# Performance work log

Hardware: AMD Instinct MI355X
Metric: run time of the kernel (lower is better)

## Reference

```python
import jax, jax.numpy as jnp
import numpy as np

H, DK, DV = 16, 64, 64
DECAY = 0.99
WRITE_STRENGTH = 1.0


def setup_inputs() -> dict:
    key = jax.random.key(0)
    ks = jax.random.split(key, 7)
    B, S, D = 4, 4096, 2048
    sd = 1.0 / np.sqrt(D)
    return {
        "hidden": jax.random.normal(ks[0], (B, S, D), jnp.float32),
        "memory": jax.random.normal(ks[1], (H, DK, DV), jnp.float32) * 0.02,
        "Wk": jax.random.normal(ks[2], (H * DK, D), jnp.float32) * sd,
        "Wv": jax.random.normal(ks[3], (H * DV, D), jnp.float32) * sd,
        "Wq": jax.random.normal(ks[4], (H * DK, D), jnp.float32) * sd,
        "Wg": jax.random.normal(ks[5], (D, D), jnp.float32) * sd,
        "Wo": jax.random.normal(ks[6], (D, H * DV), jnp.float32) * (1.0 / np.sqrt(H * DV)),
    }


def reference(hidden, memory, Wk, Wv, Wq, Wg, Wo):
    B, S, D = hidden.shape
    # projections (Linear, bias=False): x @ W^T
    k = (hidden @ Wk.T).reshape(B, S, H, DK)
    v = (hidden @ Wv.T).reshape(B, S, H, DV)
    q = (hidden @ Wq.T).reshape(B, S, H, DK)
    # read with pre-update memory: r = q^T M
    readout = jnp.einsum('bshk,hkv->bshv', q, memory).reshape(B, S, H * DV)
    # output gate: h' = h + sigmoid(Wg h) * (Wo r)
    gate = jax.nn.sigmoid(hidden @ Wg.T)
    out = hidden + gate * (readout @ Wo.T)
    # decaying outer-product write: M' = lambda*M + rho * sum_i k_i v_i^T
    new_memory = DECAY * memory + WRITE_STRENGTH * jnp.einsum('bshk,bshv->hkv', k, v)
    return out, new_memory
```

## Files before the change

kernel.cpp:

```cpp
#include <hip/hip_runtime.h>
#include <hip/hip_bf16.h>

typedef __attribute__((ext_vector_type(4))) float f32x4;
typedef __bf16 bf16x8 __attribute__((ext_vector_type(8)));

#define TOKENS 16384
#define DIM    2048
#define NKVQ   3072

__device__ __forceinline__ void gload_lds16(const void* g, void* l) {
  __builtin_amdgcn_global_load_lds((const __attribute__((address_space(1))) void*)g,
                                   (__attribute__((address_space(3))) void*)l, 16, 0, 0);
}

__device__ __forceinline__ unsigned short bfbits(float x) {
  __bf16 b = (__bf16)x; return __builtin_bit_cast(unsigned short, b);
}

__global__ void cast8_kernel(const float* __restrict__ src, __bf16* __restrict__ dst, int n8) {
  int i = blockIdx.x * blockDim.x + threadIdx.x;
  if (i >= n8) return;
  const float4* s = (const float4*)src;
  float4 a = s[2 * i], b = s[2 * i + 1];
  bf16x8 o;
  o[0] = (__bf16)a.x; o[1] = (__bf16)a.y; o[2] = (__bf16)a.z; o[3] = (__bf16)a.w;
  o[4] = (__bf16)b.x; o[5] = (__bf16)b.y; o[6] = (__bf16)b.z; o[7] = (__bf16)b.w;
  ((bf16x8*)dst)[i] = o;
}

__global__ void weff_kernel(const float* __restrict__ Wo, const float* __restrict__ mem,
                            __bf16* __restrict__ Weff) {
  int idx = blockIdx.x * blockDim.x + threadIdx.x;
  int d = idx >> 10, hk = idx & 1023, h = hk >> 6;
  const float* wo = Wo + d * 1024 + h * 64;
  const float* mm = mem + hk * 64;
  float s = 0.f;
  #pragma unroll 8
  for (int v = 0; v < 64; ++v) s += wo[v] * mm[v];
  Weff[idx] = (__bf16)s;
}

__device__ __forceinline__ void gemm256_core(
    const __bf16* __restrict__ A, int lda,
    const __bf16* __restrict__ B, int ldb,
    int m0, int n0, int nt, char* sm, f32x4 acc[8][4]) {

  const int tid = threadIdx.x, lane = tid & 63, wid = tid >> 6;
  const int wr = wid >> 2, wc = wid & 3;
  const int lrow = lane & 15, kc = lane >> 4;

  int offA[8], offB[4];
  #pragma unroll
  for (int m = 0; m < 8; ++m) {
    int u = (wr * 128 + m * 16 + lrow) * 4 + kc;
    offA[m] = (u ^ ((u >> 3) & 7)) << 4;
  }
  #pragma unroll
  for (int n = 0; n < 4; ++n) {
    int u = (wc * 64 + n * 16 + lrow) * 4 + kc;
    offB[n] = ((u ^ ((u >> 3) & 7)) << 4) + 16384;
  }

  const __bf16* pSA[2]; const __bf16* pSB[2];
  #pragma unroll
  for (int s = 0; s < 2; ++s) {
    int U = s * 512 + tid;
    int u = U ^ ((U >> 3) & 7);
    pSA[s] = A + (size_t)(m0 + (u >> 2)) * lda + (u & 3) * 8;
    pSB[s] = B + (size_t)(n0 + (u >> 2)) * ldb + (u & 3) * 8;
  }

  bf16x8 bvS0[4], bvS1[4];

#define BARX() asm volatile("s_barrier" ::: "memory")
#define VM4()  asm volatile("s_waitcnt vmcnt(4)" ::: "memory")
#define VM0()  asm volatile("s_waitcnt vmcnt(0)" ::: "memory")
#define NOVM
#define NOSTAGE
#define STAGE(bb, tt) do { \
    char* sA = sm + (bb) * 32768 + tid * 16; \
    gload_lds16(pSA[0] + (tt) * 32, sA); \
    gload_lds16(pSA[1] + (tt) * 32, sA + 8192); \
    gload_lds16(pSB[0] + (tt) * 32, sA + 16384); \
    gload_lds16(pSB[1] + (tt) * 32, sA + 24576); } while (0)

#define PH(bufC, bufN, C, N, STG, WT) do { \
    const char* bC = sm + (bufC) * 32768; \
    const char* bN = sm + (bufN) * 32768; \
    bf16x8 av[8]; \
    _Pragma("unroll") for (int m = 0; m < 8; ++m) av[m] = *(const bf16x8*)(bC + offA[m]); \
    _Pragma("unroll") for (int n = 0; n < 4; ++n) bvS##N[n] = *(const bf16x8*)(bN + offB[n]); \
    STG; \
    __builtin_amdgcn_s_setprio(1); \
    _Pragma("unroll") for (int m = 0; m < 8; ++m) \
      _Pragma("unroll") for (int n = 0; n < 4; ++n) \
        acc[m][n] = __builtin_amdgcn_mfma_f32_16x16x32_bf16(av[m], bvS##C[n], acc[m][n], 0, 0, 0); \
    __builtin_amdgcn_s_setprio(0); \
    WT; BARX(); } while (0)

#define PHF(bufC, C) do { \
    const char* bC = sm + (bufC) * 32768; \
    bf16x8 av[8]; \
    _Pragma("unroll") for (int m = 0; m < 8; ++m) av[m] = *(const bf16x8*)(bC + offA[m]); \
    __builtin_amdgcn_s_setprio(1); \
    _Pragma("unroll") for (int m = 0; m < 8; ++m) \
      _Pragma("unroll") for (int n = 0; n < 4; ++n) \
        acc[m][n] = __builtin_amdgcn_mfma_f32_16x16x32_bf16(av[m], bvS##C[n], acc[m][n], 0, 0, 0); \
    __builtin_amdgcn_s_setprio(0); } while (0)

  STAGE(0, 0); STAGE(1, 1); STAGE(2, 2);
  VM4(); BARX();
  #pragma unroll
  for (int n = 0; n < 4; ++n) bvS0[n] = *(const bf16x8*)(sm + offB[n]);

  for (int i = 0, e = (nt - 4) >> 2; i < e; ++i) {
    const int t = i << 2;
    PH(0, 1, 0, 1, STAGE(3, t + 3), VM4());
    PH(1, 2, 1, 0, STAGE(0, t + 4), VM4());
    PH(2, 3, 0, 1, STAGE(1, t + 5), VM4());
    PH(3, 0, 1, 0, STAGE(2, t + 6), VM4());
  }
  PH(0, 1, 0, 1, STAGE(3, nt - 1), VM4());
  PH(1, 2, 1, 0, NOSTAGE, VM0());
  PH(2, 3, 0, 1, NOSTAGE, NOVM);
  PHF(3, 1);
#undef PH
#undef PHF
#undef STAGE
#undef BARX
#undef VM4
#undef VM0
#undef NOVM
#undef NOSTAGE
}

__global__ void __launch_bounds__(512, 1)
gemm_fused_kernel(const __bf16* __restrict__ Xb, const __bf16* __restrict__ W1,
                  __bf16* __restrict__ Y, __bf16* __restrict__ Gb) {
  __shared__ __attribute__((aligned(16))) char smem[131072];
  const int g = (blockIdx.x & 7) * 160 + (blockIdx.x >> 3);
  const int bm = g / 20, bn = g % 20;
  const int m0 = bm * 256, n0 = bn * 256;
  f32x4 acc[8][4] = {};
  gemm256_core(Xb, DIM, W1, DIM, m0, n0, 64, smem, acc);

  const int tid = threadIdx.x, wid = tid >> 6, lane = tid & 63;
  const int wr = wid >> 2, wc = wid & 3;
  const int crow = (lane >> 4) << 2, ccol = lane & 15;
  if (bn < 12) {
    #pragma unroll
    for (int f = 0; f < 8; ++f) {
      int row = m0 + wr * 128 + f * 16 + crow;
      #pragma unroll
      for (int n = 0; n < 4; ++n) {
        int col = n0 + wc * 64 + n * 16 + ccol;
        #pragma unroll
        for (int j = 0; j < 4; ++j)
          __builtin_nontemporal_store(bfbits(acc[f][n][j]),
              (unsigned short*)(Y + (size_t)(row + j) * NKVQ + col));
      }
    }
  } else {
    const int c0 = n0 - 3072;
    #pragma unroll
    for (int f = 0; f < 8; ++f) {
      int row = m0 + wr * 128 + f * 16 + crow;
      #pragma unroll
      for (int n = 0; n < 4; ++n) {
        int col = c0 + wc * 64 + n * 16 + ccol;
        #pragma unroll
        for (int j = 0; j < 4; ++j) {
          float gv = 1.0f / (1.0f + __expf(-acc[f][n][j]));
          __builtin_nontemporal_store(bfbits(gv),
              (unsigned short*)(Gb + (size_t)(row + j) * DIM + col));
        }
      }
    }
  }
}

__global__ void __launch_bounds__(512, 1)
gemm_read_kernel(const __bf16* __restrict__ Yq, const __bf16* __restrict__ Weff,
                 const __bf16* __restrict__ Gb, const float* __restrict__ hidden,
                 float* __restrict__ out) {
  __shared__ __attribute__((aligned(16))) char smem[131072];
  const int g = (blockIdx.x & 7) * 64 + (blockIdx.x >> 3);
  const int bm = g >> 3, bn = g & 7;
  const int m0 = bm * 256, n0 = bn * 256;
  f32x4 acc[8][4] = {};
  gemm256_core(Yq, NKVQ, Weff, 1024, m0, n0, 32, smem, acc);

  const int tid = threadIdx.x, wid = tid >> 6, lane = tid & 63;
  const int wr = wid >> 2, wc = wid & 3;
  const int crow = (lane >> 4) << 2, ccol = lane & 15;
  #pragma unroll
  for (int f = 0; f < 8; ++f) {
    int row = m0 + wr * 128 + f * 16 + crow;
    #pragma unroll
    for (int n = 0; n < 4; ++n) {
      int col = n0 + wc * 64 + n * 16 + ccol;
      #pragma unroll
      for (int j = 0; j < 4; ++j) {
        size_t idx = (size_t)(row + j) * DIM + col;
        float v = hidden[idx] + (float)Gb[idx] * acc[f][n][j];
        __builtin_nontemporal_store(v, out + idx);
      }
    }
  }
}

__global__ void __launch_bounds__(256)
mem_update_kernel(const __bf16* __restrict__ Y, float* __restrict__ part) {
  const int h = blockIdx.x & 15, sp = blockIdx.x >> 4;
  __shared__ __attribute__((aligned(16))) __bf16 KT[64 * 32];
  __shared__ __attribute__((aligned(16))) __bf16 VT[64 * 32];
  const int tid = threadIdx.x, wid = tid >> 6, lane = tid & 63;
  const int lrow = lane & 15, lk = (lane >> 4) * 8;
  const __bf16* Kbase = Y + (size_t)sp * 1024 * NKVQ + h * 64;
  const __bf16* Vbase = Kbase + 1024;
  f32x4 acc[4] = {};
  const int t = tid >> 3, c8 = (tid & 7) * 8;
  for (int t0 = 0; t0 < 1024; t0 += 32) {
    __syncthreads();
    bf16x8 kv = *(const bf16x8*)(Kbase + (size_t)(t0 + t) * NKVQ + c8);
    bf16x8 vv = *(const bf16x8*)(Vbase + (size_t)(t0 + t) * NKVQ + c8);
    #pragma unroll
    for (int j = 0; j < 8; ++j) {
      KT[(c8 + j) * 32 + t] = kv[j];
      VT[(c8 + j) * 32 + t] = vv[j];
    }
    __syncthreads();
    bf16x8 af = *(const bf16x8*)(KT + (wid * 16 + lrow) * 32 + lk);
    #pragma unroll
    for (int n = 0; n < 4; ++n) {
      bf16x8 bf_ = *(const bf16x8*)(VT + (n * 16 + lrow) * 32 + lk);
      acc[n] = __builtin_amdgcn_mfma_f32_16x16x32_bf16(af, bf_, acc[n], 0, 0, 0);
    }
  }
  float* pp = part + ((size_t)sp * 16 + h) * 4096;
  const int crow = wid * 16 + (lane >> 4) * 4, ccol = lane & 15;
  #pragma unroll
  for (int n = 0; n < 4; ++n)
    #pragma unroll
    for (int r = 0; r < 4; ++r)
      pp[(crow + r) * 64 + n * 16 + ccol] = acc[n][r];
}

__global__ void mem_reduce_kernel(const float* __restrict__ part, const float* __restrict__ mem,
                                  float* __restrict__ out) {
  int i = blockIdx.x * blockDim.x + threadIdx.x;
  float s = 0.99f * mem[i];
  #pragma unroll
  for (int sp = 0; sp < 16; ++sp) s += part[sp * 65536 + i];
  out[i] = s;
}

extern "C" void kernel_launch(void* const* d_in, const int* in_sizes, int n_in,
                              void* d_out, int out_size, void* d_ws, size_t ws_size,
                              hipStream_t stream) {
  const float* hidden = (const float*)d_in[0];
  const float* memory = (const float*)d_in[1];
  const float* Wk = (const float*)d_in[2];
  const float* Wv = (const float*)d_in[3];
  const float* Wq = (const float*)d_in[4];
  const float* Wg = (const float*)d_in[5];
  const float* Wo = (const float*)d_in[6];
  float* out = (float*)d_out;
  float* mem_out = out + (size_t)TOKENS * DIM;

  char* ws = (char*)d_ws;
  __bf16* Xb   = (__bf16*)(ws);
  __bf16* W1   = (__bf16*)(ws + 67108864);
  __bf16* Weff = (__bf16*)(ws + 88080384);
  __bf16* Yb   = (__bf16*)(ws + 92274688);
  __bf16* Gb   = (__bf16*)(ws + 192937984);
  float*  part = (float*)(ws + 260046848);

  cast8_kernel<<<16384, 256, 0, stream>>>(hidden, Xb, 4194304);
  cast8_kernel<<<1024, 256, 0, stream>>>(Wk, W1, 262144);
  cast8_kernel<<<1024, 256, 0, stream>>>(Wv, W1 + 2097152, 262144);
  cast8_kernel<<<1024, 256, 0, stream>>>(Wq, W1 + 4194304, 262144);
  cast8_kernel<<<2048, 256, 0, stream>>>(Wg, W1 + 6291456, 524288);
  weff_kernel<<<8192, 256, 0, stream>>>(Wo, memory, Weff);

  gemm_fused_kernel<<<1280, 512, 0, stream>>>(Xb, W1, Yb, Gb);
  gemm_read_kernel<<<512, 512, 0, stream>>>(Yb + 2048, Weff, Gb, hidden, out);

  mem_update_kernel<<<256, 256, 0, stream>>>(Yb, part);
  mem_reduce_kernel<<<256, 256, 0, stream>>>(part, memory, mem_out);
}
```

Measured before the change: 661.1 us.

## Stage fused GEMM epilogue through LDS for vectorized stores and remap tile order

The fused projection GEMM epilogue now writes its bf16 results (with the sigmoid applied for gate tiles) into a swizzled LDS tile, then reads 16-byte rows back and issues coalesced 128-bit nontemporal stores instead of scattered 2-byte stores. Both GEMMs change their block-to-tile mapping so each XCD-strided group covers 8 adjacent M tiles sharing the same N column, aiming at better L2 reuse of weights. The read kernel drops the nontemporal hint on its fp32 output stores. The LDS round trip adds an extra barrier and shared-memory traffic.

New measurement: 630.2 us. -4.7%, faster.

```diff
diff --git a/kernel.cpp b/kernel.cpp
--- a/kernel.cpp
+++ b/kernel.cpp
@@ -3,6 +3,7 @@
 
 typedef __attribute__((ext_vector_type(4))) float f32x4;
 typedef __bf16 bf16x8 __attribute__((ext_vector_type(8)));
+typedef int int4v __attribute__((ext_vector_type(4)));
 
 #define TOKENS 16384
 #define DIM    2048
@@ -11,10 +12,6 @@
 __device__ __forceinline__ void gload_lds16(const void* g, void* l) {
   __builtin_amdgcn_global_load_lds((const __attribute__((address_space(1))) void*)g,
                                    (__attribute__((address_space(3))) void*)l, 16, 0, 0);
-}
-
-__device__ __forceinline__ unsigned short bfbits(float x) {
-  __bf16 b = (__bf16)x; return __builtin_bit_cast(unsigned short, b);
 }
 
 __global__ void cast8_kernel(const float* __restrict__ src, __bf16* __restrict__ dst, int n8) {
@@ -138,43 +135,49 @@
 gemm_fused_kernel(const __bf16* __restrict__ Xb, const __bf16* __restrict__ W1,
                   __bf16* __restrict__ Y, __bf16* __restrict__ Gb) {
   __shared__ __attribute__((aligned(16))) char smem[131072];
-  const int g = (blockIdx.x & 7) * 160 + (blockIdx.x >> 3);
-  const int bm = g / 20, bn = g % 20;
+  const int x = blockIdx.x & 7;
+  const int l = blockIdx.x >> 3;
+  const int bm = x * 8 + (l & 7);
+  const int bn = l >> 3;
   const int m0 = bm * 256, n0 = bn * 256;
   f32x4 acc[8][4] = {};
   gemm256_core(Xb, DIM, W1, DIM, m0, n0, 64, smem, acc);
 
+  __syncthreads();
   const int tid = threadIdx.x, wid = tid >> 6, lane = tid & 63;
   const int wr = wid >> 2, wc = wid & 3;
   const int crow = (lane >> 4) << 2, ccol = lane & 15;
-  if (bn < 12) {
-    #pragma unroll
-    for (int f = 0; f < 8; ++f) {
-      int row = m0 + wr * 128 + f * 16 + crow;
+  const bool isY = bn < 12;
+  #pragma unroll
+  for (int f = 0; f < 8; ++f)
+    #pragma unroll
+    for (int n = 0; n < 4; ++n)
       #pragma unroll
-      for (int n = 0; n < 4; ++n) {
-        int col = n0 + wc * 64 + n * 16 + ccol;
-        #pragma unroll
-        for (int j = 0; j < 4; ++j)
-          __builtin_nontemporal_store(bfbits(acc[f][n][j]),
-              (unsigned short*)(Y + (size_t)(row + j) * NKVQ + col));
+      for (int j = 0; j < 4; ++j) {
+        int r = wr * 128 + f * 16 + crow + j;
+        int c = wc * 64 + n * 16 + ccol;
+        float v = acc[f][n][j];
+        if (!isY) v = 1.0f / (1.0f + __expf(-v));
+        *(__bf16*)(smem + r * 512 + ((c * 2) ^ ((r & 7) << 4))) = (__bf16)v;
       }
+  __syncthreads();
+  const int rsub = tid >> 5, ch = tid & 31;
+  if (isY) {
+    #pragma unroll
+    for (int p = 0; p < 16; ++p) {
+      int r = p * 16 + rsub;
+      bf16x8 v = *(const bf16x8*)(smem + r * 512 + ((ch * 16) ^ ((r & 7) << 4)));
+      __builtin_nontemporal_store(__builtin_bit_cast(int4v, v),
+          (int4v*)(Y + (size_t)(m0 + r) * NKVQ + n0 + ch * 8));
     }
   } else {
     const int c0 = n0 - 3072;
     #pragma unroll
-    for (int f = 0; f < 8; ++f) {
-      int row = m0 + wr * 128 + f * 16 + crow;
-      #pragma unroll
-      for (int n = 0; n < 4; ++n) {
-        int col = c0 + wc * 64 + n * 16 + ccol;
-        #pragma unroll
-        for (int j = 0; j < 4; ++j) {
-          float gv = 1.0f / (1.0f + __expf(-acc[f][n][j]));
-          __builtin_nontemporal_store(bfbits(gv),
-              (unsigned short*)(Gb + (size_t)(row + j) * DIM + col));
-        }
-      }
+    for (int p = 0; p < 16; ++p) {
+      int r = p * 16 + rsub;
+      bf16x8 v = *(const bf16x8*)(smem + r * 512 + ((ch * 16) ^ ((r & 7) << 4)));
+      __builtin_nontemporal_store(__builtin_bit_cast(int4v, v),
+          (int4v*)(Gb + (size_t)(m0 + r) * DIM + c0 + ch * 8));
     }
   }
 }
@@ -184,8 +187,10 @@
                  const __bf16* __restrict__ Gb, const float* __restrict__ hidden,
                  float* __restrict__ out) {
   __shared__ __attribute__((aligned(16))) char smem[131072];
-  const int g = (blockIdx.x & 7) * 64 + (blockIdx.x >> 3);
-  const int bm = g >> 3, bn = g & 7;
+  const int x = blockIdx.x & 7;
+  const int l = blockIdx.x >> 3;
+  const int bm = x * 8 + (l & 7);
+  const int bn = l >> 3;
   const int m0 = bm * 256, n0 = bn * 256;
   f32x4 acc[8][4] = {};
   gemm256_core(Yq, NKVQ, Weff, 1024, m0, n0, 32, smem, acc);
@@ -202,8 +207,7 @@
       #pragma unroll
       for (int j = 0; j < 4; ++j) {
         size_t idx = (size_t)(row + j) * DIM + col;
-        float v = hidden[idx] + (float)Gb[idx] * acc[f][n][j];
-        __builtin_nontemporal_store(v, out + idx);
+        out[idx] = hidden[idx] + (float)Gb[idx] * acc[f][n][j];
       }
     }
   }
```
